# Kernel tuning notes

Hardware: AMD Instinct MI355X
Metric: run time of the kernel (lower is better)

Reference implementation:

```python
import jax, jax.numpy as jnp
import numpy as np

N_CODEBOOKS = 9
CODEBOOK_SIZE = 1024
CODEBOOK_DIM = 8
INPUT_DIM = 128
B, T = 16, 4096


def setup_inputs() -> dict:
    key = jax.random.key(0)
    ks = jax.random.split(key, 7)
    x = jax.random.normal(ks[0], (B, 2 * INPUT_DIM, T), dtype=jnp.float32)
    noise = jax.random.normal(ks[1], (B, INPUT_DIM, T), dtype=jnp.float32)
    # per-codebook params (stacked over the quantizer axis)
    in_w = jax.random.normal(ks[2], (N_CODEBOOKS, CODEBOOK_DIM, INPUT_DIM), dtype=jnp.float32) * 0.08
    in_b = jax.random.normal(ks[3], (N_CODEBOOKS, CODEBOOK_DIM), dtype=jnp.float32) * 0.01
    codebook = jax.random.normal(ks[4], (N_CODEBOOKS, CODEBOOK_SIZE, CODEBOOK_DIM), dtype=jnp.float32)
    out_w = jax.random.normal(ks[5], (N_CODEBOOKS, INPUT_DIM, CODEBOOK_DIM), dtype=jnp.float32) * 0.08
    out_b = jax.random.normal(ks[6], (N_CODEBOOKS, INPUT_DIM), dtype=jnp.float32) * 0.01
    return {"x": x, "noise": noise, "in_w": in_w, "in_b": in_b,
            "codebook": codebook, "out_w": out_w, "out_b": out_b}


def _l2norm(v, eps=1e-12):
    n = jnp.linalg.norm(v, axis=-1, keepdims=True)
    return v / jnp.maximum(n, eps)


def reference(x, noise, in_w, in_b, codebook, out_w, out_b):
    # --- vae_sample ---
    mean, scale = jnp.split(x, 2, axis=1)
    stdev = jax.nn.softplus(scale) + 1e-4
    var = stdev * stdev
    kl = jnp.mean(jnp.sum(mean * mean + var - jnp.log(var) - 1.0, axis=1))
    z = noise * stdev + mean  # [B, D, T]

    # --- ResidualVectorQuantize (eval mode, all codebooks) ---
    residual = z
    z_q = jnp.zeros_like(z)
    commitment_loss = jnp.float32(0.0)
    codebook_loss = jnp.float32(0.0)
    codes, lats = [], []
    b, _, t = z.shape
    for i in range(N_CODEBOOKS):
        # in_proj (1x1 conv)
        z_e = jnp.einsum("cd,bdt->bct", in_w[i], residual) + in_b[i][None, :, None]
        enc = z_e.transpose(0, 2, 1).reshape(b * t, CODEBOOK_DIM)
        enc_n = _l2norm(enc)
        cb_n = _l2norm(codebook[i])
        # squared L2 distance between normalized vectors
        dist = (jnp.sum(enc_n * enc_n, axis=1, keepdims=True)
                - 2.0 * enc_n @ cb_n.T
                + jnp.sum(cb_n * cb_n, axis=1)[None, :])
        idx = jnp.argmin(dist, axis=1).reshape(b, t)  # [B, T]
        zq_i = codebook[i][idx].transpose(0, 2, 1)  # [B, c, T] (raw codebook)
        # mse_loss(...).mean([1,2]).mean() == global mean
        commitment_loss = commitment_loss + jnp.mean((z_e - jax.lax.stop_gradient(zq_i)) ** 2)
        codebook_loss = codebook_loss + jnp.mean((zq_i - jax.lax.stop_gradient(z_e)) ** 2)
        # straight-through estimator
        zq_st = z_e + jax.lax.stop_gradient(zq_i - z_e)
        out = jnp.einsum("dc,bct->bdt", out_w[i], zq_st) + out_b[i][None, :, None]
        z_q = z_q + out
        residual = residual - out
        codes.append(idx)
        lats.append(z_e)
    codes = jnp.stack(codes, axis=1)          # [B, N, T]
    latents = jnp.concatenate(lats, axis=1)   # [B, N*c, T]
    commitment_loss = commitment_loss / N_CODEBOOKS
    codebook_loss = codebook_loss / N_CODEBOOKS
    return z_q, kl, commitment_loss, codebook_loss, codes, latents
```

## Files before the change

### kernel.cpp

```cpp
#include <hip/hip_runtime.h>
#include <cstdint>
#include <cstddef>

constexpr int T   = 4096;
constexpr int BB  = 16;
constexpr int D   = 128;
constexpr int CB  = 1024;
constexpr int CD  = 8;
constexpr int NCB = 9;

constexpr int TBLK = 64;
constexpr int NTHR = 256;

constexpr size_t OFF_ZQ    = 0;
constexpr size_t OFF_SCAL  = (size_t)BB * D * T;
constexpr size_t OFF_CODES = OFF_SCAL + 3;
constexpr size_t OFF_LAT   = OFF_CODES + (size_t)BB * NCB * T;

constexpr size_t AFR_U32 = (size_t)NCB * 64 * 2 * 64 * 4;
constexpr size_t H2M_F32 = (size_t)NCB * 64 * 64 * 4;

typedef short bf16x8 __attribute__((ext_vector_type(8)));
typedef float f32x4  __attribute__((ext_vector_type(4)));

__device__ __forceinline__ unsigned short f2bf(float f) {
    unsigned u = __float_as_uint(f);
    return (unsigned short)((u + (((u >> 16) & 1u) + 0x7FFFu)) >> 16);
}
__device__ __forceinline__ float bf2f(unsigned short b) {
    return __uint_as_float((unsigned)b << 16);
}


__global__ void prep_kernel(const float* __restrict__ codebook,
                            unsigned* __restrict__ afr,
                            float* __restrict__ h2m,
                            float* __restrict__ scal) {
    int e = blockIdx.x * blockDim.x + threadIdx.x;
    if (e == 0) { scal[0] = 0.f; scal[1] = 0.f; scal[2] = 0.f; }
    if (e >= NCB * CB) return;
    const int i  = e >> 10;
    const int en = e & 1023;
    const int et = en >> 4;
    const int m  = en & 15;

    float v[CD]; float s2 = 0.f;
#pragma unroll
    for (int j = 0; j < CD; ++j) { v[j] = codebook[(size_t)e * CD + j]; s2 = fmaf(v[j], v[j], s2); }
    float inv = 1.0f / fmaxf(sqrtf(s2), 1e-12f);
    float cn[CD]; float c2 = 0.f;
#pragma unroll
    for (int j = 0; j < CD; ++j) { cn[j] = v[j] * inv; c2 = fmaf(cn[j], cn[j], c2); }
    float nh2 = -0.5f * c2;

    {
        size_t base = (((size_t)i * 64 + et) * 64 + (size_t)(m >> 2) * 16) * 4 + (m & 3);
        for (int nl2 = 0; nl2 < 16; ++nl2) h2m[base + (size_t)nl2 * 4] = nh2;
    }

    unsigned pk[3][4];
#pragma unroll
    for (int w = 0; w < 4; ++w) {
        float x0 = cn[2 * w], x1 = cn[2 * w + 1];
        unsigned short a0 = f2bf(x0); float r0 = x0 - bf2f(a0);
        unsigned short a1 = f2bf(r0); float q0 = r0 - bf2f(a1);
        unsigned short a2 = f2bf(q0);
        unsigned short b0 = f2bf(x1); float r1 = x1 - bf2f(b0);
        unsigned short b1 = f2bf(r1); float q1 = r1 - bf2f(b1);
        unsigned short b2 = f2bf(q1);
        pk[0][w] = (unsigned)a0 | ((unsigned)b0 << 16);
        pk[1][w] = (unsigned)a1 | ((unsigned)b1 << 16);
        pk[2][w] = (unsigned)a2 | ((unsigned)b2 << 16);
    }

    const int At[8] = {0, 1, 2, 0, 1, 0, 2, 1};
#pragma unroll
    for (int kh = 0; kh < 2; ++kh) {
#pragma unroll
        for (int h = 0; h < 4; ++h) {
            int A1 = At[kh * 4 + (h >> 1)];
            int A2 = At[kh * 4 + 2 + (h >> 1)];
            int dw = (h & 1) * 2;
            size_t off = ((((size_t)i * 64 + et) * 2 + kh) * 64 + (h * 16 + m)) * 4;
            afr[off + 0] = pk[A1][dw];
            afr[off + 1] = pk[A1][dw + 1];
            afr[off + 2] = pk[A2][dw];
            afr[off + 3] = pk[A2][dw + 1];
        }
    }
}

__global__ __launch_bounds__(NTHR, 4)
void rvq_kernel(const float* __restrict__ x,
                const float* __restrict__ noise,
                const float* __restrict__ in_w,
                const float* __restrict__ in_b,
                const float* __restrict__ codebook,
                const float* __restrict__ out_w,
                const float* __restrict__ out_b,
                const unsigned* __restrict__ afr,
                const float* __restrict__ h2m,
                float* __restrict__ o_zq,
                float* __restrict__ o_scal,
                float* __restrict__ o_codes,
                float* __restrict__ o_lat) {
    __shared__ float    res[D * TBLK];
    __shared__ float    zen[TBLK * 9];
    __shared__ unsigned es[TBLK * 12];
    __shared__ float    redS[4 * TBLK];
    __shared__ int      redI[4 * TBLK];
    __shared__ float    redw[8];

    const int tid = threadIdx.x;
    const int c   = tid & 63;
    const int s   = tid >> 6;
    const int su  = __builtin_amdgcn_readfirstlane(s);
    const int b   = blockIdx.x >> 6;
    const int t0  = (blockIdx.x & 63) << 6;
    const int t   = t0 + c;

    const int l  = tid & 63;
    const int h  = l >> 4;
    const int nl = l & 15;

    float kl_local = 0.f;
    {
        const float* xm = x     + (size_t)b * 2 * D * T + (size_t)(su * 32) * T + t;
        const float* xs = xm    + (size_t)D * T;
        const float* nz = noise + (size_t)b * D * T     + (size_t)(su * 32) * T + t;
#pragma unroll 8
        for (int k = 0; k < 32; ++k) {
            float m  = xm[(size_t)k * T];
            float sc = xs[(size_t)k * T];
            float nv = nz[(size_t)k * T];
            float sp  = fmaxf(sc, 0.f) + log1pf(expf(-fabsf(sc)));
            float sd  = sp + 1e-4f;
            float var = sd * sd;
            float zv  = fmaf(nv, sd, m);
            res[(su * 32 + k) * TBLK + c] = zv;
            kl_local += m * m + var - logf(var) - 1.0f;
        }
    }

    float loss_local = 0.f;

    for (int i = 0; i < NCB; ++i) {
        __syncthreads();

        {
            const float* w0 = in_w + (size_t)(i * CD + su) * D;
            const float* w1 = w0 + 4 * D;
            float a0 = in_b[i * CD + su];
            float a1 = in_b[i * CD + su + 4];
#pragma unroll 16
            for (int k = 0; k < D; ++k) {
                float r = res[k * TBLK + c];
                a0 = fmaf(w0[k], r, a0);
                a1 = fmaf(w1[k], r, a1);
            }
            zen[c * 9 + su]     = a0;
            zen[c * 9 + su + 4] = a1;
            o_lat[(size_t)b * (NCB * CD) * T + (size_t)(i * CD + su) * T + t]     = a0;
            o_lat[(size_t)b * (NCB * CD) * T + (size_t)(i * CD + su + 4) * T + t] = a1;
        }
        __syncthreads();

        if (tid < 64) {
            float v[CD]; float n2 = 0.f;
#pragma unroll
            for (int j = 0; j < CD; ++j) { v[j] = zen[tid * 9 + j]; n2 = fmaf(v[j], v[j], n2); }
            float inv = 1.0f / fmaxf(sqrtf(n2), 1e-12f);
            unsigned pk[3][4];
#pragma unroll
            for (int w = 0; w < 4; ++w) {
                float x0 = v[2 * w] * inv, x1 = v[2 * w + 1] * inv;
                unsigned short a0 = f2bf(x0); float r0 = x0 - bf2f(a0);
                unsigned short a1 = f2bf(r0); float q0 = r0 - bf2f(a1);
                unsigned short a2 = f2bf(q0);
                unsigned short b0 = f2bf(x1); float r1 = x1 - bf2f(b0);
                unsigned short b1 = f2bf(r1); float q1 = r1 - bf2f(b1);
                unsigned short b2 = f2bf(q1);
                pk[0][w] = (unsigned)a0 | ((unsigned)b0 << 16);
                pk[1][w] = (unsigned)a1 | ((unsigned)b1 << 16);
                pk[2][w] = (unsigned)a2 | ((unsigned)b2 << 16);
            }
            uint4* ep = reinterpret_cast<uint4*>(&es[(size_t)tid * 12]);
            ep[0] = make_uint4(pk[0][0], pk[0][1], pk[0][2], pk[0][3]);
            ep[1] = make_uint4(pk[1][0], pk[1][1], pk[1][2], pk[1][3]);
            ep[2] = make_uint4(pk[2][0], pk[2][1], pk[2][2], pk[2][3]);
        }
        __syncthreads();

        bf16x8 bfrag[4][2];
        {
            const int dwo = (h & 1) * 2;
            const int tA  = h >> 1;
            const int tB  = 1 + (h >> 1);
#pragma unroll
            for (int pt = 0; pt < 4; ++pt) {
                const int col = pt * 16 + nl;
                uint2 lo0 = *reinterpret_cast<const uint2*>(&es[col * 12 + 0 * 4 + dwo]);
                uint2 hi0 = *reinterpret_cast<const uint2*>(&es[col * 12 + tA * 4 + dwo]);
                uint2 lh1 = *reinterpret_cast<const uint2*>(&es[col * 12 + tB * 4 + dwo]);
                uint4 t0v = make_uint4(lo0.x, lo0.y, hi0.x, hi0.y);
                uint4 t1v = make_uint4(lh1.x, lh1.y, lh1.x, lh1.y);
                bfrag[pt][0] = *reinterpret_cast<bf16x8*>(&t0v);
                bfrag[pt][1] = *reinterpret_cast<bf16x8*>(&t1v);
            }
        }

        float best[4] = {-3.0e38f, -3.0e38f, -3.0e38f, -3.0e38f};
        int   bidx[4] = {0, 0, 0, 0};
        {
            const uint4* Ab = reinterpret_cast<const uint4*>(afr)
                              + ((size_t)(i * 64 + su * 16) * 2) * 64 + l;
            const f32x4* Hb = reinterpret_cast<const f32x4*>(h2m)
                              + (size_t)(i * 64 + su * 16) * 64 + l;
            int eb = (su * 16) * 16 + h * 4;
#pragma unroll 2
            for (int e16 = 0; e16 < 16; ++e16) {
                uint4 ua0 = Ab[0];
                uint4 ua1 = Ab[64];
                f32x4 hv  = Hb[0];
                bf16x8 a0 = *reinterpret_cast<bf16x8*>(&ua0);
                bf16x8 a1 = *reinterpret_cast<bf16x8*>(&ua1);
#pragma unroll
                for (int pt = 0; pt < 4; ++pt) {
                    f32x4 acc = __builtin_amdgcn_mfma_f32_16x16x32_bf16(a0, bfrag[pt][0], hv, 0, 0, 0);
                    acc = __builtin_amdgcn_mfma_f32_16x16x32_bf16(a1, bfrag[pt][1], acc, 0, 0, 0);
#pragma unroll
                    for (int r = 0; r < 4; ++r) {
                        float sc = acc[r];
                        if (sc > best[pt]) { best[pt] = sc; bidx[pt] = eb + r; }
                    }
                }
                Ab += 128; Hb += 64; eb += 16;
            }
        }

#pragma unroll
        for (int off = 16; off <= 32; off <<= 1) {
#pragma unroll
            for (int pt = 0; pt < 4; ++pt) {
                float ob = __shfl_xor(best[pt], off, 64);
                int   oi = __shfl_xor(bidx[pt], off, 64);
                bool tk = (ob > best[pt]) || (ob == best[pt] && oi < bidx[pt]);
                if (tk) { best[pt] = ob; bidx[pt] = oi; }
            }
        }
        if (l < 16) {
#pragma unroll
            for (int pt = 0; pt < 4; ++pt) {
                redS[su * 64 + pt * 16 + l] = best[pt];
                redI[su * 64 + pt * 16 + l] = bidx[pt];
            }
        }
        __syncthreads();

        float bsc = redS[c];
        int   bi  = redI[c];
#pragma unroll
        for (int ww = 1; ww < 4; ++ww) {
            float v2 = redS[ww * TBLK + c];
            int   vi = redI[ww * TBLK + c];
            if (v2 > bsc) { bsc = v2; bi = vi; }
        }
        if (s == 0) o_codes[(size_t)b * NCB * T + (size_t)i * T + t] = (float)bi;

        float zq[CD];
        {
            float zer[CD];
#pragma unroll
            for (int j = 0; j < CD; ++j) zer[j] = zen[c * 9 + j];
            const float4* cr4 = (const float4*)(codebook + ((size_t)i * CB + bi) * CD);
            float4 qa = cr4[0], qb = cr4[1];
            float cv[CD] = {qa.x, qa.y, qa.z, qa.w, qb.x, qb.y, qb.z, qb.w};
#pragma unroll
            for (int j = 0; j < CD; ++j) {
                zq[j] = zer[j] + (cv[j] - zer[j]);
                if (s == 0) { float dd = cv[j] - zer[j]; loss_local = fmaf(dd, dd, loss_local); }
            }
        }

        {
            const float* ow = out_w + (size_t)(i * D + su * 32) * CD;
            const float* ob = out_b + i * D + su * 32;
#pragma unroll 4
            for (int k = 0; k < 32; ++k) {
                float acc = ob[k];
#pragma unroll
                for (int j = 0; j < CD; ++j) acc = fmaf(ow[k * CD + j], zq[j], acc);
                res[(su * 32 + k) * TBLK + c] -= acc;
            }
        }
    }
    __syncthreads();

    {
        const float* xm = x     + (size_t)b * 2 * D * T + (size_t)(su * 32) * T + t;
        const float* xs = xm    + (size_t)D * T;
        const float* nz = noise + (size_t)b * D * T     + (size_t)(su * 32) * T + t;
        float*       oq = o_zq  + (size_t)b * D * T     + (size_t)(su * 32) * T + t;
#pragma unroll 8
        for (int k = 0; k < 32; ++k) {
            float m  = xm[(size_t)k * T];
            float sc = xs[(size_t)k * T];
            float nv = nz[(size_t)k * T];
            float sp = fmaxf(sc, 0.f) + log1pf(expf(-fabsf(sc)));
            float sd = sp + 1e-4f;
            float zv = fmaf(nv, sd, m);
            oq[(size_t)k * T] = zv - res[(su * 32 + k) * TBLK + c];
        }
    }

    float v = kl_local;
#pragma unroll
    for (int o = 32; o > 0; o >>= 1) v += __shfl_down(v, o, 64);
    float w2 = loss_local;
#pragma unroll
    for (int o = 32; o > 0; o >>= 1) w2 += __shfl_down(w2, o, 64);
    if ((tid & 63) == 0) { redw[s] = v; redw[4 + s] = w2; }
    __syncthreads();
    if (tid == 0) {
        float ks = redw[0] + redw[1] + redw[2] + redw[3];
        float ls = redw[4] + redw[5] + redw[6] + redw[7];
        atomicAdd(&o_scal[0], ks * (1.0f / 65536.0f));
        float lsn = ls * (1.0f / (524288.0f * 9.0f));
        atomicAdd(&o_scal[1], lsn);
        atomicAdd(&o_scal[2], lsn);
    }
}

extern "C" void kernel_launch(void* const* d_in, const int* in_sizes, int n_in,
                              void* d_out, int out_size, void* d_ws, size_t ws_size,
                              hipStream_t stream) {
    const float* x        = (const float*)d_in[0];
    const float* noise    = (const float*)d_in[1];
    const float* in_w     = (const float*)d_in[2];
    const float* in_b     = (const float*)d_in[3];
    const float* codebook = (const float*)d_in[4];
    const float* out_w    = (const float*)d_in[5];
    const float* out_b    = (const float*)d_in[6];

    float* out     = (float*)d_out;
    float* o_zq    = out + OFF_ZQ;
    float* o_scal  = out + OFF_SCAL;
    float* o_codes = out + OFF_CODES;
    float* o_lat   = out + OFF_LAT;

    unsigned* afr = (unsigned*)d_ws;
    float*    h2m = (float*)(afr + AFR_U32);

    prep_kernel<<<(NCB * CB + 255) / 256, 256, 0, stream>>>(codebook, afr, h2m, o_scal);

    dim3 grid(BB * (T / TBLK));
    rvq_kernel<<<grid, NTHR, 0, stream>>>(x, noise, in_w, in_b, codebook, out_w, out_b,
                                          afr, h2m, o_zq, o_scal, o_codes, o_lat);
}
```

Baseline: 394.1 us.

## Precompute all codebook latents with one MFMA projection and fold residual updates algebraically

The residual chain is rewritten algebraically. The in_proj of every codebook applied to the residual becomes an in_w projection of z computed once with split-bf16 MFMA. Each later latent is then corrected by a small precomputed 72x8 matrix (in_w·out_w) times the selected code, with the biases folded into a prep-time term. The final z_q is rebuilt by summing precomputed out_w·codebook rows gathered by code index. This removes the per-codebook 128-wide residual matmul and the second pass over x and noise, but adds a large OPt workspace table with gathers, extra prep work, and a risk of numerical drift in argmin decisions.

```diff
diff --git a/kernel.cpp b/kernel.cpp
--- a/kernel.cpp
+++ b/kernel.cpp
@@ -11,6 +11,7 @@
 
 constexpr int TBLK = 64;
 constexpr int NTHR = 256;
+constexpr int ZLS  = 66;
 
 constexpr size_t OFF_ZQ    = 0;
 constexpr size_t OFF_SCAL  = (size_t)BB * D * T;
@@ -18,7 +19,12 @@
 constexpr size_t OFF_LAT   = OFF_CODES + (size_t)BB * NCB * T;
 
 constexpr size_t AFR_U32 = (size_t)NCB * 64 * 2 * 64 * 4;
-constexpr size_t H2M_F32 = (size_t)NCB * 64 * 64 * 4;
+constexpr size_t H2C_F32 = (size_t)NCB * CB;
+constexpr size_t AFW_U32 = (size_t)2 * 6 * 2 * 5 * 64 * 4;
+constexpr size_t CM_F32  = (size_t)NCB * 72 * 8;
+constexpr size_t OBS_F32 = 128;
+constexpr size_t BEF_F32 = 72;
+constexpr size_t OP_F32  = (size_t)NCB * CB * D;
 
 typedef short bf16x8 __attribute__((ext_vector_type(8)));
 typedef float f32x4  __attribute__((ext_vector_type(4)));
@@ -31,85 +37,186 @@
     return __uint_as_float((unsigned)b << 16);
 }
 
+constexpr int PAIR_A[6] = {0, 0, 1, 1, 2, 0};
+constexpr int PAIR_B[6] = {0, 1, 0, 1, 0, 2};
+
+__device__ __forceinline__ unsigned short splitterm(float xv, int term) {
+    unsigned short t0 = f2bf(xv); if (term == 0) return t0;
+    float r1 = xv - bf2f(t0);
+    unsigned short t1 = f2bf(r1); if (term == 1) return t1;
+    float r2 = r1 - bf2f(t1);
+    return f2bf(r2);
+}
 
 __global__ void prep_kernel(const float* __restrict__ codebook,
+                            const float* __restrict__ in_w,
+                            const float* __restrict__ in_b,
+                            const float* __restrict__ out_w,
+                            const float* __restrict__ out_b,
                             unsigned* __restrict__ afr,
-                            float* __restrict__ h2m,
+                            float* __restrict__ h2c,
+                            unsigned* __restrict__ afw,
+                            float* __restrict__ CMt,
+                            float* __restrict__ obs,
+                            float* __restrict__ bef,
+                            float* __restrict__ OPt,
                             float* __restrict__ scal) {
-    int e = blockIdx.x * blockDim.x + threadIdx.x;
-    if (e == 0) { scal[0] = 0.f; scal[1] = 0.f; scal[2] = 0.f; }
-    if (e >= NCB * CB) return;
-    const int i  = e >> 10;
-    const int en = e & 1023;
-    const int et = en >> 4;
-    const int m  = en & 15;
-
-    float v[CD]; float s2 = 0.f;
-#pragma unroll
-    for (int j = 0; j < CD; ++j) { v[j] = codebook[(size_t)e * CD + j]; s2 = fmaf(v[j], v[j], s2); }
-    float inv = 1.0f / fmaxf(sqrtf(s2), 1e-12f);
-    float cn[CD]; float c2 = 0.f;
-#pragma unroll
-    for (int j = 0; j < CD; ++j) { cn[j] = v[j] * inv; c2 = fmaf(cn[j], cn[j], c2); }
-    float nh2 = -0.5f * c2;
-
-    {
-        size_t base = (((size_t)i * 64 + et) * 64 + (size_t)(m >> 2) * 16) * 4 + (m & 3);
-        for (int nl2 = 0; nl2 < 16; ++nl2) h2m[base + (size_t)nl2 * 4] = nh2;
-    }
-
-    unsigned pk[3][4];
-#pragma unroll
-    for (int w = 0; w < 4; ++w) {
-        float x0 = cn[2 * w], x1 = cn[2 * w + 1];
-        unsigned short a0 = f2bf(x0); float r0 = x0 - bf2f(a0);
-        unsigned short a1 = f2bf(r0); float q0 = r0 - bf2f(a1);
-        unsigned short a2 = f2bf(q0);
-        unsigned short b0 = f2bf(x1); float r1 = x1 - bf2f(b0);
-        unsigned short b1 = f2bf(r1); float q1 = r1 - bf2f(b1);
-        unsigned short b2 = f2bf(q1);
-        pk[0][w] = (unsigned)a0 | ((unsigned)b0 << 16);
-        pk[1][w] = (unsigned)a1 | ((unsigned)b1 << 16);
-        pk[2][w] = (unsigned)a2 | ((unsigned)b2 << 16);
-    }
-
-    const int At[8] = {0, 1, 2, 0, 1, 0, 2, 1};
-#pragma unroll
-    for (int kh = 0; kh < 2; ++kh) {
-#pragma unroll
-        for (int h = 0; h < 4; ++h) {
-            int A1 = At[kh * 4 + (h >> 1)];
-            int A2 = At[kh * 4 + 2 + (h >> 1)];
-            int dw = (h & 1) * 2;
-            size_t off = ((((size_t)i * 64 + et) * 2 + kh) * 64 + (h * 16 + m)) * 4;
-            afr[off + 0] = pk[A1][dw];
-            afr[off + 1] = pk[A1][dw + 1];
-            afr[off + 2] = pk[A2][dw];
-            afr[off + 3] = pk[A2][dw + 1];
-        }
+    const int gid = blockIdx.x * blockDim.x + threadIdx.x;
+    if (gid == 0) { scal[0] = 0.f; scal[1] = 0.f; scal[2] = 0.f; }
+
+    if (gid < NCB * CB) {
+        const int e  = gid;
+        const int i  = e >> 10;
+        const int en = e & 1023;
+        const int et = en >> 4;
+        const int m  = en & 15;
+
+        float v[CD]; float s2 = 0.f;
+#pragma unroll
+        for (int j = 0; j < CD; ++j) { v[j] = codebook[(size_t)e * CD + j]; s2 = fmaf(v[j], v[j], s2); }
+        float inv = 1.0f / fmaxf(sqrtf(s2), 1e-12f);
+        float cn[CD]; float c2 = 0.f;
+#pragma unroll
+        for (int j = 0; j < CD; ++j) { cn[j] = v[j] * inv; c2 = fmaf(cn[j], cn[j], c2); }
+        h2c[e] = -0.5f * c2;
+
+        unsigned pk[3][4];
+#pragma unroll
+        for (int w = 0; w < 4; ++w) {
+            float x0 = cn[2 * w], x1 = cn[2 * w + 1];
+            unsigned short a0 = f2bf(x0); float r0 = x0 - bf2f(a0);
+            unsigned short a1 = f2bf(r0); float q0 = r0 - bf2f(a1);
+            unsigned short a2 = f2bf(q0);
+            unsigned short b0 = f2bf(x1); float r1 = x1 - bf2f(b0);
+            unsigned short b1 = f2bf(r1); float q1 = r1 - bf2f(b1);
+            unsigned short b2 = f2bf(q1);
+            pk[0][w] = (unsigned)a0 | ((unsigned)b0 << 16);
+            pk[1][w] = (unsigned)a1 | ((unsigned)b1 << 16);
+            pk[2][w] = (unsigned)a2 | ((unsigned)b2 << 16);
+        }
+        const int At[8] = {0, 1, 2, 0, 1, 0, 2, 1};
+#pragma unroll
+        for (int kh = 0; kh < 2; ++kh) {
+#pragma unroll
+            for (int h = 0; h < 4; ++h) {
+                int A1 = At[kh * 4 + (h >> 1)];
+                int A2 = At[kh * 4 + 2 + (h >> 1)];
+                int dw = (h & 1) * 2;
+                size_t off = ((((size_t)i * 64 + et) * 2 + kh) * 64 + (h * 16 + m)) * 4;
+                afr[off + 0] = pk[A1][dw];
+                afr[off + 1] = pk[A1][dw + 1];
+                afr[off + 2] = pk[A2][dw];
+                afr[off + 3] = pk[A2][dw + 1];
+            }
+        }
+        return;
+    }
+    if (gid < 2 * NCB * CB) {
+        const int e = gid - NCB * CB;
+        const int i = e >> 10;
+        float cv[CD];
+#pragma unroll
+        for (int d = 0; d < CD; ++d) cv[d] = codebook[(size_t)e * CD + d];
+        const float* ow = out_w + (size_t)i * D * CD;
+        float* dst = OPt + (size_t)e * D;
+        for (int r = 0; r < D; ++r) {
+            float a = 0.f;
+#pragma unroll
+            for (int d = 0; d < CD; ++d) a = fmaf(ow[r * CD + d], cv[d], a);
+            dst[r] = a;
+        }
+        return;
+    }
+    if (gid < 2 * NCB * CB + NCB * 72) {
+        const int idx = gid - 2 * NCB * CB;
+        const int j = idx / 72, r = idx - j * 72;
+        const float* wi = in_w + (size_t)r * D;
+        const float* ow = out_w + (size_t)j * D * CD;
+        float a[CD];
+#pragma unroll
+        for (int d = 0; d < CD; ++d) a[d] = 0.f;
+        for (int k = 0; k < D; ++k) {
+            float w = wi[k];
+#pragma unroll
+            for (int d = 0; d < CD; ++d) a[d] = fmaf(w, ow[k * CD + d], a[d]);
+        }
+#pragma unroll
+        for (int d = 0; d < CD; ++d) CMt[((size_t)j * 72 + r) * CD + d] = a[d];
+        return;
+    }
+    if (gid < 2 * NCB * CB + NCB * 72 + 128) {
+        const int r = gid - (2 * NCB * CB + NCB * 72);
+        float a = 0.f;
+        for (int i = 0; i < NCB; ++i) a += out_b[(size_t)i * D + r];
+        obs[r] = a;
+        return;
+    }
+    if (gid < 2 * NCB * CB + NCB * 72 + 128 + 72) {
+        const int row = gid - (2 * NCB * CB + NCB * 72 + 128);
+        const int ic  = row >> 3;
+        const float* wi = in_w + (size_t)row * D;
+        float a = in_b[row];
+        for (int j = 0; j < ic; ++j) {
+            const float* ob = out_b + (size_t)j * D;
+            float s = 0.f;
+            for (int k = 0; k < D; ++k) s = fmaf(wi[k], ob[k], s);
+            a -= s;
+        }
+        bef[row] = a;
+        return;
+    }
+    if (gid < 2 * NCB * CB + NCB * 72 + 128 + 72 + 7680) {
+        int idx = gid - (2 * NCB * CB + NCB * 72 + 128 + 72);
+        const int lane = idx & 63; idx >>= 6;
+        const int mt = idx % 5; idx /= 5;
+        const int kq = idx & 1; idx >>= 1;
+        const int p  = idx % 6;
+        const int P  = idx / 6;
+        const int h  = lane >> 4, m = lane & 15;
+        const int row = mt * 16 + m;
+        const int term = PAIR_A[p];
+        const int D0 = P * 64 + kq * 32 + h * 4;
+        const int doff[4][2] = {{0, 1}, {2, 3}, {16, 17}, {18, 19}};
+        unsigned wv[4];
+#pragma unroll
+        for (int w = 0; w < 4; ++w) {
+            unsigned short lo = 0, hi = 0;
+            if (row < 72) {
+                lo = splitterm(in_w[(size_t)row * D + D0 + doff[w][0]], term);
+                hi = splitterm(in_w[(size_t)row * D + D0 + doff[w][1]], term);
+            }
+            wv[w] = (unsigned)lo | ((unsigned)hi << 16);
+        }
+        *reinterpret_cast<uint4*>(afw + ((size_t)(((P * 6 + p) * 2 + kq) * 5 + mt) * 64 + lane) * 4)
+            = make_uint4(wv[0], wv[1], wv[2], wv[3]);
+        return;
     }
 }
 
 __global__ __launch_bounds__(NTHR, 4)
 void rvq_kernel(const float* __restrict__ x,
                 const float* __restrict__ noise,
-                const float* __restrict__ in_w,
-                const float* __restrict__ in_b,
                 const float* __restrict__ codebook,
-                const float* __restrict__ out_w,
-                const float* __restrict__ out_b,
                 const unsigned* __restrict__ afr,
-                const float* __restrict__ h2m,
+                const float* __restrict__ h2c,
+                const unsigned* __restrict__ afw,
+                const float* __restrict__ CMt,
+                const float* __restrict__ obs,
+                const float* __restrict__ bef,
+                const float* __restrict__ OPt,
                 float* __restrict__ o_zq,
                 float* __restrict__ o_scal,
                 float* __restrict__ o_codes,
                 float* __restrict__ o_lat) {
-    __shared__ float    res[D * TBLK];
-    __shared__ float    zen[TBLK * 9];
+    __shared__ char     zbuf[24576];
     __shared__ unsigned es[TBLK * 12];
     __shared__ float    redS[4 * TBLK];
     __shared__ int      redI[4 * TBLK];
+    __shared__ int      cidx[NCB * TBLK];
     __shared__ float    redw[8];
+
+    uint2* zs = reinterpret_cast<uint2*>(zbuf);
+    float* Zl = reinterpret_cast<float*>(zbuf);
 
     const int tid = threadIdx.x;
     const int c   = tid & 63;
@@ -124,51 +231,93 @@
     const int nl = l & 15;
 
     float kl_local = 0.f;
-    {
-        const float* xm = x     + (size_t)b * 2 * D * T + (size_t)(su * 32) * T + t;
-        const float* xs = xm    + (size_t)D * T;
-        const float* nz = noise + (size_t)b * D * T     + (size_t)(su * 32) * T + t;
-#pragma unroll 8
-        for (int k = 0; k < 32; ++k) {
-            float m  = xm[(size_t)k * T];
-            float sc = xs[(size_t)k * T];
-            float nv = nz[(size_t)k * T];
-            float sp  = fmaxf(sc, 0.f) + log1pf(expf(-fabsf(sc)));
-            float sd  = sp + 1e-4f;
-            float var = sd * sd;
-            float zv  = fmaf(nv, sd, m);
-            res[(su * 32 + k) * TBLK + c] = zv;
-            kl_local += m * m + var - logf(var) - 1.0f;
-        }
-    }
+    f32x4 acc[5];
+#pragma unroll
+    for (int mt = 0; mt < 5; ++mt) {
+        int row0 = mt * 16 + h * 4;
+        if (row0 < 72) acc[mt] = *reinterpret_cast<const f32x4*>(bef + row0);
+        else           acc[mt] = f32x4{0.f, 0.f, 0.f, 0.f};
+    }
+
+#pragma unroll 1
+    for (int P = 0; P < 2; ++P) {
+        {
+            const int r0 = P * 64 + su * 16;
+            const float* xm = x     + (size_t)b * 2 * D * T + (size_t)r0 * T + t;
+            const float* xs = xm    + (size_t)D * T;
+            const float* nz = noise + (size_t)b * D * T     + (size_t)r0 * T + t;
+            float zrow[16];
+#pragma unroll
+            for (int k = 0; k < 16; ++k) {
+                float m  = xm[(size_t)k * T];
+                float sc = xs[(size_t)k * T];
+                float nv = nz[(size_t)k * T];
+                float sp  = fmaxf(sc, 0.f) + log1pf(expf(-fabsf(sc)));
+                float sd  = sp + 1e-4f;
+                float var = sd * sd;
+                zrow[k]   = fmaf(nv, sd, m);
+                kl_local += m * m + var - logf(var) - 1.0f;
+            }
+#pragma unroll
+            for (int db = 0; db < 4; ++db) {
+                unsigned w[3][2];
+#pragma unroll
+                for (int half = 0; half < 2; ++half) {
+                    float x0 = zrow[db * 4 + half * 2], x1 = zrow[db * 4 + half * 2 + 1];
+                    unsigned short a0 = f2bf(x0); float r1 = x0 - bf2f(a0);
+                    unsigned short a1 = f2bf(r1); float r2 = r1 - bf2f(a1);
+                    unsigned short a2 = f2bf(r2);
+                    unsigned short b0 = f2bf(x1); float s1v = x1 - bf2f(b0);
+                    unsigned short b1 = f2bf(s1v); float s2v = s1v - bf2f(b1);
+                    unsigned short b2 = f2bf(s2v);
+                    w[0][half] = (unsigned)a0 | ((unsigned)b0 << 16);
+                    w[1][half] = (unsigned)a1 | ((unsigned)b1 << 16);
+                    w[2][half] = (unsigned)a2 | ((unsigned)b2 << 16);
+                }
+#pragma unroll
+                for (int tt = 0; tt < 3; ++tt)
+                    zs[(tt * 16 + su * 4 + db) * 64 + c] = make_uint2(w[tt][0], w[tt][1]);
+            }
+        }
+        __syncthreads();
+        {
+            const int colB = su * 16 + nl;
+#pragma unroll
+            for (int p = 0; p < 6; ++p) {
+#pragma unroll
+                for (int kq = 0; kq < 2; ++kq) {
+                    uint2 blo = zs[(PAIR_B[p] * 16 + kq * 8 + h) * 64 + colB];
+                    uint2 bhi = zs[(PAIR_B[p] * 16 + kq * 8 + 4 + h) * 64 + colB];
+                    uint4 bu = make_uint4(blo.x, blo.y, bhi.x, bhi.y);
+                    bf16x8 bfr = *reinterpret_cast<bf16x8*>(&bu);
+                    const uint4* Aw = reinterpret_cast<const uint4*>(afw)
+                                      + (size_t)(((P * 6 + p) * 2 + kq) * 5) * 64 + l;
+#pragma unroll
+                    for (int mt = 0; mt < 5; ++mt) {
+                        uint4 au = Aw[(size_t)mt * 64];
+                        bf16x8 af = *reinterpret_cast<bf16x8*>(&au);
+                        acc[mt] = __builtin_amdgcn_mfma_f32_16x16x32_bf16(af, bfr, acc[mt], 0, 0, 0);
+                    }
+                }
+            }
+        }
+        __syncthreads();
+    }
+#pragma unroll
+    for (int mt = 0; mt < 5; ++mt)
+#pragma unroll
+        for (int r = 0; r < 4; ++r)
+            Zl[(mt * 16 + h * 4 + r) * ZLS + su * 16 + nl] = acc[mt][r];
 
     float loss_local = 0.f;
 
     for (int i = 0; i < NCB; ++i) {
         __syncthreads();
 
-        {
-            const float* w0 = in_w + (size_t)(i * CD + su) * D;
-            const float* w1 = w0 + 4 * D;
-            float a0 = in_b[i * CD + su];
-            float a1 = in_b[i * CD + su + 4];
-#pragma unroll 16
-            for (int k = 0; k < D; ++k) {
-                float r = res[k * TBLK + c];
-                a0 = fmaf(w0[k], r, a0);
-                a1 = fmaf(w1[k], r, a1);
-            }
-            zen[c * 9 + su]     = a0;
-            zen[c * 9 + su + 4] = a1;
-            o_lat[(size_t)b * (NCB * CD) * T + (size_t)(i * CD + su) * T + t]     = a0;
-            o_lat[(size_t)b * (NCB * CD) * T + (size_t)(i * CD + su + 4) * T + t] = a1;
-        }
-        __syncthreads();
-
         if (tid < 64) {
             float v[CD]; float n2 = 0.f;
 #pragma unroll
-            for (int j = 0; j < CD; ++j) { v[j] = zen[tid * 9 + j]; n2 = fmaf(v[j], v[j], n2); }
+            for (int j = 0; j < CD; ++j) { v[j] = Zl[(i * CD + j) * ZLS + tid]; n2 = fmaf(v[j], v[j], n2); }
             float inv = 1.0f / fmaxf(sqrtf(n2), 1e-12f);
             unsigned pk[3][4];
 #pragma unroll
@@ -189,6 +338,12 @@
             ep[1] = make_uint4(pk[1][0], pk[1][1], pk[1][2], pk[1][3]);
             ep[2] = make_uint4(pk[2][0], pk[2][1], pk[2][2], pk[2][3]);
         }
+        {
+            float la0 = Zl[(i * CD + su) * ZLS + c];
+            float la1 = Zl[(i * CD + su + 4) * ZLS + c];
+            o_lat[(size_t)b * (NCB * CD) * T + (size_t)(i * CD + su) * T + t]     = la0;
+            o_lat[(size_t)b * (NCB * CD) * T + (size_t)(i * CD + su + 4) * T + t] = la1;
+        }
         __syncthreads();
 
         bf16x8 bfrag[4][2];
@@ -214,27 +369,26 @@
         {
             const uint4* Ab = reinterpret_cast<const uint4*>(afr)
                               + ((size_t)(i * 64 + su * 16) * 2) * 64 + l;
-            const f32x4* Hb = reinterpret_cast<const f32x4*>(h2m)
-                              + (size_t)(i * 64 + su * 16) * 64 + l;
+            const f32x4* Hb = reinterpret_cast<const f32x4*>(h2c + (size_t)i * CB + su * 256);
             int eb = (su * 16) * 16 + h * 4;
 #pragma unroll 2
             for (int e16 = 0; e16 < 16; ++e16) {
                 uint4 ua0 = Ab[0];
                 uint4 ua1 = Ab[64];
-                f32x4 hv  = Hb[0];
+                f32x4 hv  = Hb[e16 * 4 + h];
                 bf16x8 a0 = *reinterpret_cast<bf16x8*>(&ua0);
                 bf16x8 a1 = *reinterpret_cast<bf16x8*>(&ua1);
 #pragma unroll
                 for (int pt = 0; pt < 4; ++pt) {
-                    f32x4 acc = __builtin_amdgcn_mfma_f32_16x16x32_bf16(a0, bfrag[pt][0], hv, 0, 0, 0);
-                    acc = __builtin_amdgcn_mfma_f32_16x16x32_bf16(a1, bfrag[pt][1], acc, 0, 0, 0);
+                    f32x4 accd = __builtin_amdgcn_mfma_f32_16x16x32_bf16(a0, bfrag[pt][0], hv, 0, 0, 0);
+                    accd = __builtin_amdgcn_mfma_f32_16x16x32_bf16(a1, bfrag[pt][1], accd, 0, 0, 0);
 #pragma unroll
                     for (int r = 0; r < 4; ++r) {
-                        float sc = acc[r];
+                        float sc = accd[r];
                         if (sc > best[pt]) { best[pt] = sc; bidx[pt] = eb + r; }
                     }
                 }
-                Ab += 128; Hb += 64; eb += 16;
+                Ab += 128; eb += 16;
             }
         }
 
@@ -265,52 +419,56 @@
             int   vi = redI[ww * TBLK + c];
             if (v2 > bsc) { bsc = v2; bi = vi; }
         }
+        cidx[i * TBLK + c] = bi;
         if (s == 0) o_codes[(size_t)b * NCB * T + (size_t)i * T + t] = (float)bi;
 
-        float zq[CD];
-        {
-            float zer[CD];
-#pragma unroll
-            for (int j = 0; j < CD; ++j) zer[j] = zen[c * 9 + j];
+        float cv[CD];
+        {
             const float4* cr4 = (const float4*)(codebook + ((size_t)i * CB + bi) * CD);
             float4 qa = cr4[0], qb = cr4[1];
-            float cv[CD] = {qa.x, qa.y, qa.z, qa.w, qb.x, qb.y, qb.z, qb.w};
-#pragma unroll
-            for (int j = 0; j < CD; ++j) {
-                zq[j] = zer[j] + (cv[j] - zer[j]);
-                if (s == 0) { float dd = cv[j] - zer[j]; loss_local = fmaf(dd, dd, loss_local); }
-            }
-        }
-
-        {
-            const float* ow = out_w + (size_t)(i * D + su * 32) * CD;
-            const float* ob = out_b + i * D + su * 32;
-#pragma unroll 4
-            for (int k = 0; k < 32; ++k) {
-                float acc = ob[k];
-#pragma unroll
-                for (int j = 0; j < CD; ++j) acc = fmaf(ow[k * CD + j], zq[j], acc);
-                res[(su * 32 + k) * TBLK + c] -= acc;
+            cv[0] = qa.x; cv[1] = qa.y; cv[2] = qa.z; cv[3] = qa.w;
+            cv[4] = qb.x; cv[5] = qb.y; cv[6] = qb.z; cv[7] = qb.w;
+            if (s == 0) {
+#pragma unroll
+                for (int j = 0; j < CD; ++j) {
+                    float dd = cv[j] - Zl[(i * CD + j) * ZLS + c];
+                    loss_local = fmaf(dd, dd, loss_local);
+                }
+            }
+        }
+
+        {
+            const int nf = 64 - 8 * i;
+            for (int rr = su; rr < nf; rr += 4) {
+                const int row = (i + 1) * 8 + rr;
+                float zv = Zl[row * ZLS + c];
+                const float* cm = CMt + ((size_t)i * 72 + row) * CD;
+#pragma unroll
+                for (int d2 = 0; d2 < CD; ++d2) zv = fmaf(-cm[d2], cv[d2], zv);
+                Zl[row * ZLS + c] = zv;
             }
         }
     }
     __syncthreads();
 
     {
-        const float* xm = x     + (size_t)b * 2 * D * T + (size_t)(su * 32) * T + t;
-        const float* xs = xm    + (size_t)D * T;
-        const float* nz = noise + (size_t)b * D * T     + (size_t)(su * 32) * T + t;
-        float*       oq = o_zq  + (size_t)b * D * T     + (size_t)(su * 32) * T + t;
-#pragma unroll 8
-        for (int k = 0; k < 32; ++k) {
-            float m  = xm[(size_t)k * T];
-            float sc = xs[(size_t)k * T];
-            float nv = nz[(size_t)k * T];
-            float sp = fmaxf(sc, 0.f) + log1pf(expf(-fabsf(sc)));
-            float sd = sp + 1e-4f;
-            float zv = fmaf(nv, sd, m);
-            oq[(size_t)k * T] = zv - res[(su * 32 + k) * TBLK + c];
-        }
+        f32x4 oa[8];
+#pragma unroll
+        for (int kb = 0; kb < 8; ++kb)
+            oa[kb] = *reinterpret_cast<const f32x4*>(obs + su * 32 + kb * 4);
+#pragma unroll
+        for (int i2 = 0; i2 < NCB; ++i2) {
+            int code = cidx[i2 * TBLK + c];
+            const f32x4* op = reinterpret_cast<const f32x4*>(OPt + ((size_t)(i2 * CB + code)) * D + su * 32);
+#pragma unroll
+            for (int kb = 0; kb < 8; ++kb) oa[kb] += op[kb];
+        }
+        float* oq = o_zq + (size_t)b * D * T + (size_t)(su * 32) * T + t;
+#pragma unroll
+        for (int kb = 0; kb < 8; ++kb)
+#pragma unroll
+            for (int r = 0; r < 4; ++r)
+                oq[(size_t)(kb * 4 + r) * T] = oa[kb][r];
     }
 
     float v = kl_local;
@@ -349,11 +507,19 @@
     float* o_lat   = out + OFF_LAT;
 
     unsigned* afr = (unsigned*)d_ws;
-    float*    h2m = (float*)(afr + AFR_U32);
-
-    prep_kernel<<<(NCB * CB + 255) / 256, 256, 0, stream>>>(codebook, afr, h2m, o_scal);
+    float*    h2c = (float*)(afr + AFR_U32);
+    unsigned* afw = (unsigned*)(h2c + H2C_F32);
+    float*    CMt = (float*)(afw + AFW_U32);
+    float*    obs = CMt + CM_F32;
+    float*    bef = obs + OBS_F32;
+    float*    OPt = bef + BEF_F32;
+
+    const int prep_total = 2 * NCB * CB + NCB * 72 + 128 + 72 + 7680;
+    prep_kernel<<<(prep_total + 255) / 256, 256, 0, stream>>>(
+        codebook, in_w, in_b, out_w, out_b, afr, h2c, afw, CMt, obs, bef, OPt, o_scal);
 
     dim3 grid(BB * (T / TBLK));
-    rvq_kernel<<<grid, NTHR, 0, stream>>>(x, noise, in_w, in_b, codebook, out_w, out_b,
-                                          afr, h2m, o_zq, o_scal, o_codes, o_lat);
+    rvq_kernel<<<grid, NTHR, 0, stream>>>(x, noise, codebook,
+                                          afr, h2c, afw, CMt, obs, bef, OPt,
+                                          o_zq, o_scal, o_codes, o_lat);
 }
```

After: 389.0 us. No clear change (-1.3%).
